# Kernel tuning notes

Measured on AMD Instinct MI355X. Metric: run time of the kernel, lower is better.

The kernel has to match this reference:

```python
import jax, jax.numpy as jnp
import numpy as np
import math

B, T, D_MODEL, H = 2, 2048, 768, 12
D = D_MODEL // H
EPS = 1e-8


def _l2norm(x, eps=EPS):
    # torch.nn.functional.normalize: x / max(||x||, eps)
    n = jnp.sqrt(jnp.sum(x * x, axis=-1, keepdims=True))
    return x / jnp.maximum(n, eps)


def setup_inputs() -> dict:
    key = jax.random.key(0)
    ks = jax.random.split(key, 7)
    sc = 1.0 / math.sqrt(D_MODEL)
    inp = {
        "query": jax.random.normal(ks[0], (B, T, D_MODEL), jnp.float32),
        "key": jax.random.normal(ks[1], (B, T, D_MODEL), jnp.float32),
        "value": jax.random.normal(ks[2], (B, T, D_MODEL), jnp.float32),
        "Wq": jax.random.normal(ks[3], (D_MODEL, D_MODEL), jnp.float32) * sc,
        "Wk": jax.random.normal(ks[4], (D_MODEL, D_MODEL), jnp.float32) * sc,
        "Wv": jax.random.normal(ks[5], (D_MODEL, D_MODEL), jnp.float32) * sc,
        "Wo": jax.random.normal(ks[6], (D_MODEL, D_MODEL), jnp.float32) * sc,
        "s_v": jnp.linspace(0.0, math.log(255.0), H).astype(jnp.float32),
        "s_r": jnp.zeros((H,), jnp.float32),
    }
    return inp


def reference(query, key, value, Wq, Wk, Wv, Wo, s_v, s_r):
    b, t, _ = query.shape

    def proj(x, W):  # Linear(bias=False) then split heads -> [B,H,T,D]
        return (x @ W.T).reshape(b, t, H, D).transpose(0, 2, 1, 3)

    q = _l2norm(proj(query, Wq))
    k = _l2norm(proj(key, Wk))
    v = _l2norm(proj(value, Wv))

    w = jnp.exp(s_v) + 1.0  # per-head decay exponent, in [2, 256]
    r = jnp.exp(s_r) + 1.0  # per-head scale

    # cosine-similarity scores in [-1, 1]
    s = jnp.einsum("bhqd,bhkd->bhqk", q, k)
    base = jnp.clip((s + 1.0) * 0.5, 0.0, 1.0)
    alpha = r[None, :, None, None] * jnp.power(base, w[None, :, None, None])

    # causal mask (no softmax normalization in screening attention)
    causal = jnp.tril(jnp.ones((t, t), dtype=bool))
    alpha = jnp.where(causal[None, None], alpha, 0.0)

    out = jnp.einsum("bhqk,bhkd->bhqd", alpha, v)  # [B,H,T,D]

    # TanhNorm: bound magnitude along head dim via tanh of the norm
    n = jnp.sqrt(jnp.sum(out * out, axis=-1, keepdims=True))
    out = jnp.tanh(n) * out / (n + EPS)

    out = out.transpose(0, 2, 1, 3).reshape(b, t, D_MODEL)
    return out @ Wo.T
```

## Files before the change

### kernel.cpp

```cpp
#include <hip/hip_runtime.h>
#include <hip/hip_bf16.h>
#include <math.h>


typedef __attribute__((ext_vector_type(8))) short short8;
typedef __attribute__((ext_vector_type(4))) float f32x4;
typedef __attribute__((ext_vector_type(4))) unsigned int uint4v;
typedef __attribute__((ext_vector_type(2))) unsigned int uint2v;
typedef __attribute__((ext_vector_type(4))) float float4v;

#define MFMA_BF16(a, b, c) __builtin_amdgcn_mfma_f32_16x16x32_bf16((a), (b), (c), 0, 0, 0)

static __device__ __forceinline__ unsigned short f2bf(float f) {
  union { float f; unsigned u; } v; v.f = f;
  unsigned r = v.u + 0x7FFFu + ((v.u >> 16) & 1u);
  return (unsigned short)(r >> 16);
}
static __device__ __forceinline__ unsigned pack2(float a, float b) {
  return (unsigned)f2bf(a) | ((unsigned)f2bf(b) << 16);
}
static __device__ __forceinline__ void gload_lds16(const void* g, void* l) {
  __builtin_amdgcn_global_load_lds((const __attribute__((address_space(1))) unsigned int*)g,
                                   (__attribute__((address_space(3))) unsigned int*)l, 16, 0, 0);
}

__global__ __launch_bounds__(256) void k_cvt(
    const float* __restrict__ s0, const float* __restrict__ s1, const float* __restrict__ s2,
    const float* __restrict__ s3, const float* __restrict__ s4, const float* __restrict__ s5,
    const float* __restrict__ s6, unsigned short* __restrict__ dst) {
  const size_t e = ((size_t)blockIdx.x * 256 + threadIdx.x) * 8;
  const float* src;
  size_t off;
  if (e < 9437184) {
    const int i = (int)(e / 3145728);
    src = (i == 0) ? s0 : (i == 1) ? s1 : s2;
    off = e - (size_t)i * 3145728;
  } else {
    const size_t ew = e - 9437184;
    const int i = (int)(ew / 589824);
    src = (i == 0) ? s3 : (i == 1) ? s4 : (i == 2) ? s5 : s6;
    off = ew - (size_t)i * 589824;
  }
  const float4v f0 = *(const float4v*)(src + off);
  const float4v f1 = *(const float4v*)(src + off + 4);
  uint4v u = {pack2(f0.x, f0.y), pack2(f0.z, f0.w), pack2(f1.x, f1.y), pack2(f1.z, f1.w)};
  *(uint4v*)(dst + e) = u;
}

__global__ __launch_bounds__(512) void k_proj(
    const unsigned short* __restrict__ Xb, const unsigned short* __restrict__ Wb,
    unsigned short* __restrict__ qb, unsigned short* __restrict__ kb,
    unsigned short* __restrict__ vtb) {
  __shared__ alignas(16) unsigned char smem[49152];
  float* o_s = (float*)smem;
  unsigned short* vt_s = (unsigned short*)smem;

  const int which = blockIdx.z;
  const int h = blockIdx.y;
  const unsigned short* X = Xb + (size_t)which * 3145728;
  const unsigned short* W = Wb + (size_t)which * 589824 + (size_t)h * 64 * 768;

  const int mbase = blockIdx.x * 128;
  const int tid = threadIdx.x;
  const int lane = tid & 63;
  const int wv = tid >> 6;
  const int wm = wv >> 1, wn = wv & 1;
  const int l15 = lane & 15, l4 = lane >> 4;
  const int srow8 = lane >> 3;
  const int schunk = (lane & 7) ^ srow8;

  f32x4 acc[2][2];
#pragma unroll
  for (int m = 0; m < 2; ++m)
#pragma unroll
    for (int n = 0; n < 2; ++n) acc[m][n] = (f32x4){0.f, 0.f, 0.f, 0.f};

#pragma unroll
  for (int i = 0; i < 2; ++i) {
    const int j = wv * 2 + i;
    gload_lds16(X + (size_t)(mbase + j * 8 + srow8) * 768 + schunk * 8, smem + j * 1024);
  }
  gload_lds16(W + (size_t)(wv * 8 + srow8) * 768 + schunk * 8, smem + 16384 + wv * 1024);

  for (int ks = 0; ks < 12; ++ks) {
    const int cur = (ks & 1) * 24576;
    asm volatile("s_waitcnt vmcnt(0)" ::: "memory");
    __builtin_amdgcn_sched_barrier(0);
    __builtin_amdgcn_s_barrier();
    __builtin_amdgcn_sched_barrier(0);
    if (ks < 11) {
      const int nxt = ((ks + 1) & 1) * 24576;
      const int k0n = (ks + 1) * 64;
#pragma unroll
      for (int i = 0; i < 2; ++i) {
        const int j = wv * 2 + i;
        gload_lds16(X + (size_t)(mbase + j * 8 + srow8) * 768 + k0n + schunk * 8,
                    smem + nxt + j * 1024);
      }
      gload_lds16(W + (size_t)(wv * 8 + srow8) * 768 + k0n + schunk * 8,
                  smem + nxt + 16384 + wv * 1024);
      __builtin_amdgcn_sched_barrier(0);
    }
    __builtin_amdgcn_s_setprio(1);
#pragma unroll
    for (int kc = 0; kc < 2; ++kc) {
      const int cx = (kc << 2) | l4;
      short8 ar[2], br[2];
#pragma unroll
      for (int m = 0; m < 2; ++m) {
        const int r = wm * 32 + m * 16 + l15;
        ar[m] = *(const short8*)(smem + cur + r * 128 + ((cx ^ (r & 7)) << 4));
      }
#pragma unroll
      for (int n = 0; n < 2; ++n) {
        const int r = wn * 32 + n * 16 + l15;
        br[n] = *(const short8*)(smem + cur + 16384 + r * 128 + ((cx ^ (r & 7)) << 4));
      }
#pragma unroll
      for (int m = 0; m < 2; ++m)
#pragma unroll
        for (int n = 0; n < 2; ++n) acc[m][n] = MFMA_BF16(ar[m], br[n], acc[m][n]);
    }
    __builtin_amdgcn_s_setprio(0);
  }

  const int b = mbase >> 11;
  const int tbase = mbase & 2047;
  const int bh = b * 12 + h;
  __syncthreads();
#pragma unroll
  for (int m = 0; m < 2; ++m)
#pragma unroll
    for (int n = 0; n < 2; ++n)
#pragma unroll
      for (int j = 0; j < 4; ++j)
        o_s[(wm * 32 + m * 16 + l4 * 4 + j) * 68 + wn * 32 + n * 16 + l15] = acc[m][n][j];
  __syncthreads();
  const int row2 = tid >> 2, q4 = tid & 3;
  float v[16];
  float ss = 0.f;
#pragma unroll
  for (int c = 0; c < 4; ++c) {
    float4v f = *(const float4v*)(o_s + row2 * 68 + q4 * 16 + c * 4);
    v[c * 4 + 0] = f.x; v[c * 4 + 1] = f.y; v[c * 4 + 2] = f.z; v[c * 4 + 3] = f.w;
    ss += f.x * f.x + f.y * f.y + f.z * f.z + f.w * f.w;
  }
  ss += __shfl_xor(ss, 1);
  ss += __shfl_xor(ss, 2);
  const float inv = 1.f / fmaxf(sqrtf(ss), 1e-8f);
  if (which < 2) {
    unsigned short* outp =
        ((which == 0) ? qb : kb) + ((size_t)bh * 2048 + tbase + row2) * 64 + q4 * 16;
    uint4v o0 = {pack2(v[0] * inv, v[1] * inv), pack2(v[2] * inv, v[3] * inv),
                 pack2(v[4] * inv, v[5] * inv), pack2(v[6] * inv, v[7] * inv)};
    uint4v o1 = {pack2(v[8] * inv, v[9] * inv), pack2(v[10] * inv, v[11] * inv),
                 pack2(v[12] * inv, v[13] * inv), pack2(v[14] * inv, v[15] * inv)};
    *(uint4v*)(outp) = o0;
    *(uint4v*)(outp + 8) = o1;
  } else {
    __syncthreads();
#pragma unroll
    for (int c = 0; c < 16; ++c)
      vt_s[(q4 * 16 + c) * 136 + row2] = f2bf(v[c] * inv);
    __syncthreads();
    const int d = tid >> 3, tc = (tid & 7) * 16;
    unsigned short* dst = vtb + ((size_t)bh * 64 + d) * 2048 + tbase + tc;
    *(uint4v*)(dst) = *(const uint4v*)(vt_s + d * 136 + tc);
    *(uint4v*)(dst + 8) = *(const uint4v*)(vt_s + d * 136 + tc + 8);
  }
}

__global__ __launch_bounds__(512) void k_attn(
    const unsigned short* __restrict__ qb, const unsigned short* __restrict__ kb,
    const unsigned short* __restrict__ vtb, const float* __restrict__ s_v,
    const float* __restrict__ s_r, unsigned short* __restrict__ attn) {
  __shared__ alignas(16) unsigned char smem[41984];
  unsigned short* p_s = (unsigned short*)(smem + 32768);
  float* o_s = (float*)smem;

  const int bid = blockIdx.x;
  const int ii = bid & 255, jj = bid >> 8;
  const int rank = (jj == 0) ? ii : (jj == 1) ? (511 - ii) : (512 + ii);
  const int qt = 31 - (rank / 24);
  const int bh = rank % 24;
  const int b = bh / 12, h = bh % 12;
  const int qbase = qt * 64;
  const unsigned short* Qp = qb + (size_t)bh * 2048 * 64;
  const unsigned short* Kp = kb + (size_t)bh * 2048 * 64;
  const unsigned short* VTp = vtb + (size_t)bh * 64 * 2048;

  const int tid = threadIdx.x;
  const int lane = tid & 63;
  const int wv = tid >> 6;
  const int wm = wv >> 2, wn = wv & 3;
  const int l15 = lane & 15, l4 = lane >> 4;
  const int srow8 = lane >> 3;
  const int schunk = (lane & 7) ^ srow8;

  const float w_h = expf(s_v[h]) + 1.0f;
  const float lr_h = log2f(expf(s_r[h]) + 1.0f);

  gload_lds16(Kp + (size_t)(wv * 8 + srow8) * 64 + schunk * 8, smem + wv * 1024);
  gload_lds16(VTp + (size_t)(wv * 8 + srow8) * 2048 + schunk * 8, smem + 16384 + wv * 1024);

  short8 qf[2];
#pragma unroll
  for (int kc = 0; kc < 2; ++kc)
    qf[kc] = *(const short8*)(Qp + (size_t)(qbase + wn * 16 + l15) * 64 + kc * 32 + l4 * 8);

  f32x4 acc_o[2];
#pragma unroll
  for (int m = 0; m < 2; ++m) acc_o[m] = (f32x4){0.f, 0.f, 0.f, 0.f};

  for (int kt = 0; kt <= qt; ++kt) {
    const int cur = (kt & 1) * 8192;
    asm volatile("s_waitcnt vmcnt(0)" ::: "memory");
    __builtin_amdgcn_sched_barrier(0);
    __builtin_amdgcn_s_barrier();
    __builtin_amdgcn_sched_barrier(0);
    if (kt < qt) {
      const int nxt = ((kt + 1) & 1) * 8192;
      const int kb2 = (kt + 1) * 64;
      gload_lds16(Kp + (size_t)(kb2 + wv * 8 + srow8) * 64 + schunk * 8, smem + nxt + wv * 1024);
      gload_lds16(VTp + (size_t)(wv * 8 + srow8) * 2048 + kb2 + schunk * 8,
                  smem + 16384 + nxt + wv * 1024);
      __builtin_amdgcn_sched_barrier(0);
    }
    f32x4 s_acc[2];
#pragma unroll
    for (int m = 0; m < 2; ++m) s_acc[m] = (f32x4){0.f, 0.f, 0.f, 0.f};
    __builtin_amdgcn_s_setprio(1);
#pragma unroll
    for (int kc = 0; kc < 2; ++kc) {
      const int cx = (kc << 2) | l4;
      const int r0 = wm * 32 + l15, r1 = wm * 32 + 16 + l15;
      short8 a0 = *(const short8*)(smem + cur + r0 * 128 + ((cx ^ (r0 & 7)) << 4));
      short8 a1 = *(const short8*)(smem + cur + r1 * 128 + ((cx ^ (r1 & 7)) << 4));
      s_acc[0] = MFMA_BF16(a0, qf[kc], s_acc[0]);
      s_acc[1] = MFMA_BF16(a1, qf[kc], s_acc[1]);
    }
    __builtin_amdgcn_s_setprio(0);
    const bool diag = (kt == qt);
#pragma unroll
    for (int m = 0; m < 2; ++m) {
      const int lkb = wm * 32 + m * 16 + l4 * 4;
      const int lq = wn * 16 + l15;
      float av[4];
#pragma unroll
      for (int t = 0; t < 4; ++t) {
        const float base = __builtin_amdgcn_fmed3f(fmaf(s_acc[m][t], 0.5f, 0.5f), 0.f, 1.f);
        float a = __builtin_amdgcn_exp2f(fmaf(w_h, __builtin_amdgcn_logf(base), lr_h));
        if (diag && (lkb + t) > lq) a = 0.f;
        av[t] = a;
      }
      uint2v u = {pack2(av[0], av[1]), pack2(av[2], av[3])};
      *(uint2v*)(p_s + lq * 72 + lkb) = u;
    }
    asm volatile("s_waitcnt lgkmcnt(0)" ::: "memory");
    __builtin_amdgcn_sched_barrier(0);
    __builtin_amdgcn_s_barrier();
    __builtin_amdgcn_sched_barrier(0);
    __builtin_amdgcn_s_setprio(1);
#pragma unroll
    for (int kc = 0; kc < 2; ++kc) {
      const int cx = (kc << 2) | l4;
      const int r0 = wm * 32 + l15, r1 = wm * 32 + 16 + l15;
      short8 pa = *(const short8*)(p_s + (wn * 16 + l15) * 72 + kc * 32 + l4 * 8);
      short8 vb0 = *(const short8*)(smem + 16384 + cur + r0 * 128 + ((cx ^ (r0 & 7)) << 4));
      short8 vb1 = *(const short8*)(smem + 16384 + cur + r1 * 128 + ((cx ^ (r1 & 7)) << 4));
      acc_o[0] = MFMA_BF16(pa, vb0, acc_o[0]);
      acc_o[1] = MFMA_BF16(pa, vb1, acc_o[1]);
    }
    __builtin_amdgcn_s_setprio(0);
  }
  __syncthreads();
#pragma unroll
  for (int m = 0; m < 2; ++m)
#pragma unroll
    for (int j = 0; j < 4; ++j)
      o_s[(wn * 16 + l4 * 4 + j) * 68 + wm * 32 + m * 16 + l15] = acc_o[m][j];
  __syncthreads();
  {
    const int row = tid >> 3, d8 = (tid & 7) * 8;
    float vals[8];
    float ss = 0.f;
#pragma unroll
    for (int c = 0; c < 2; ++c) {
      float4v f = *(const float4v*)(o_s + row * 68 + d8 + c * 4);
      vals[c * 4 + 0] = f.x; vals[c * 4 + 1] = f.y; vals[c * 4 + 2] = f.z; vals[c * 4 + 3] = f.w;
      ss += f.x * f.x + f.y * f.y + f.z * f.z + f.w * f.w;
    }
    ss += __shfl_xor(ss, 1);
    ss += __shfl_xor(ss, 2);
    ss += __shfl_xor(ss, 4);
    const float nrm = sqrtf(ss);
    const float sc = tanhf(nrm) / (nrm + 1e-8f);
    unsigned short* dst = attn + (size_t)(b * 2048 + qbase + row) * 768 + h * 64 + d8;
    uint4v o = {pack2(vals[0] * sc, vals[1] * sc), pack2(vals[2] * sc, vals[3] * sc),
                pack2(vals[4] * sc, vals[5] * sc), pack2(vals[6] * sc, vals[7] * sc)};
    *(uint4v*)(dst) = o;
  }
}

__global__ __launch_bounds__(512) void k_outproj(const unsigned short* __restrict__ attn,
                                                 const unsigned short* __restrict__ Wob,
                                                 float* __restrict__ out) {
  __shared__ alignas(16) unsigned char smem[49152];
  const int mbase = blockIdx.x * 128;
  const int nbase = blockIdx.y * 64;
  const int tid = threadIdx.x;
  const int lane = tid & 63;
  const int wv = tid >> 6;
  const int wm = wv >> 1, wn = wv & 1;
  const int l15 = lane & 15, l4 = lane >> 4;
  const int srow8 = lane >> 3;
  const int schunk = (lane & 7) ^ srow8;

  f32x4 acc[2][2];
#pragma unroll
  for (int m = 0; m < 2; ++m)
#pragma unroll
    for (int n = 0; n < 2; ++n) acc[m][n] = (f32x4){0.f, 0.f, 0.f, 0.f};

#pragma unroll
  for (int i = 0; i < 2; ++i) {
    const int j = wv * 2 + i;
    gload_lds16(attn + (size_t)(mbase + j * 8 + srow8) * 768 + schunk * 8, smem + j * 1024);
  }
  gload_lds16(Wob + (size_t)(nbase + wv * 8 + srow8) * 768 + schunk * 8,
              smem + 16384 + wv * 1024);

  for (int ks = 0; ks < 12; ++ks) {
    const int cur = (ks & 1) * 24576;
    asm volatile("s_waitcnt vmcnt(0)" ::: "memory");
    __builtin_amdgcn_sched_barrier(0);
    __builtin_amdgcn_s_barrier();
    __builtin_amdgcn_sched_barrier(0);
    if (ks < 11) {
      const int nxt = ((ks + 1) & 1) * 24576;
      const int k0n = (ks + 1) * 64;
#pragma unroll
      for (int i = 0; i < 2; ++i) {
        const int j = wv * 2 + i;
        gload_lds16(attn + (size_t)(mbase + j * 8 + srow8) * 768 + k0n + schunk * 8,
                    smem + nxt + j * 1024);
      }
      gload_lds16(Wob + (size_t)(nbase + wv * 8 + srow8) * 768 + k0n + schunk * 8,
                  smem + nxt + 16384 + wv * 1024);
      __builtin_amdgcn_sched_barrier(0);
    }
    __builtin_amdgcn_s_setprio(1);
#pragma unroll
    for (int kc = 0; kc < 2; ++kc) {
      const int cx = (kc << 2) | l4;
      short8 ar[2], br[2];
#pragma unroll
      for (int m = 0; m < 2; ++m) {
        const int r = wm * 32 + m * 16 + l15;
        ar[m] = *(const short8*)(smem + cur + r * 128 + ((cx ^ (r & 7)) << 4));
      }
#pragma unroll
      for (int n = 0; n < 2; ++n) {
        const int r = wn * 32 + n * 16 + l15;
        br[n] = *(const short8*)(smem + cur + 16384 + r * 128 + ((cx ^ (r & 7)) << 4));
      }
#pragma unroll
      for (int m = 0; m < 2; ++m)
#pragma unroll
        for (int n = 0; n < 2; ++n) acc[m][n] = MFMA_BF16(ar[m], br[n], acc[m][n]);
    }
    __builtin_amdgcn_s_setprio(0);
  }
#pragma unroll
  for (int m = 0; m < 2; ++m)
#pragma unroll
    for (int n = 0; n < 2; ++n)
#pragma unroll
      for (int j = 0; j < 4; ++j)
        out[(size_t)(mbase + wm * 32 + m * 16 + l4 * 4 + j) * 768 + nbase + wn * 32 + n * 16 +
            l15] = acc[m][n][j];
}

extern "C" void kernel_launch(void* const* d_in, const int* in_sizes, int n_in, void* d_out,
                              int out_size, void* d_ws, size_t ws_size, hipStream_t stream) {
  (void)in_sizes;
  (void)n_in;
  (void)out_size;
  (void)ws_size;
  const float* query = (const float*)d_in[0];
  const float* key = (const float*)d_in[1];
  const float* value = (const float*)d_in[2];
  const float* Wq = (const float*)d_in[3];
  const float* Wk = (const float*)d_in[4];
  const float* Wv = (const float*)d_in[5];
  const float* Wo = (const float*)d_in[6];
  const float* s_v = (const float*)d_in[7];
  const float* s_r = (const float*)d_in[8];
  float* out = (float*)d_out;

  unsigned short* cvt = (unsigned short*)d_ws;
  unsigned short* Xb = cvt;
  unsigned short* Wb = cvt + 9437184;
  unsigned short* qb = cvt + 11796480;
  unsigned short* kb = qb + 3145728;
  unsigned short* vtb = kb + 3145728;
  unsigned short* attn = cvt;

  k_cvt<<<5760, 256, 0, stream>>>(query, key, value, Wq, Wk, Wv, Wo, cvt);
  k_proj<<<dim3(32, 12, 3), 512, 0, stream>>>(Xb, Wb, qb, kb, vtb);
  k_attn<<<dim3(768), 512, 0, stream>>>(qb, kb, vtb, s_v, s_r, attn);
  k_outproj<<<dim3(32, 12), 512, 0, stream>>>(attn, Wb + 3 * 589824, out);
}
```

Before: 79.76 us.

## Split PV over key halves per wave to drop the mid-loop barrier

The PV product is reorganized so each wave uses only the P columns it wrote itself (its key half wm) and covers all 64 head dims with transposed accumulators. This lets the block-wide barrier between writing P and reading it be removed. The two key-half partial outputs are then summed through shared memory at the end, which costs an extra barrier pass and more accumulator registers. Correctness relies on each wave reading only P entries from its own writes, which the layout appears to ensure.

```diff
diff --git a/kernel.cpp b/kernel.cpp
--- a/kernel.cpp
+++ b/kernel.cpp
@@ -208,9 +208,9 @@
   for (int kc = 0; kc < 2; ++kc)
     qf[kc] = *(const short8*)(Qp + (size_t)(qbase + wn * 16 + l15) * 64 + kc * 32 + l4 * 8);
 
-  f32x4 acc_o[2];
-#pragma unroll
-  for (int m = 0; m < 2; ++m) acc_o[m] = (f32x4){0.f, 0.f, 0.f, 0.f};
+  f32x4 acc_oT[4];
+#pragma unroll
+  for (int g = 0; g < 4; ++g) acc_oT[g] = (f32x4){0.f, 0.f, 0.f, 0.f};
 
   for (int kt = 0; kt <= qt; ++kt) {
     const int cur = (kt & 1) * 8192;
@@ -258,27 +258,35 @@
     }
     asm volatile("s_waitcnt lgkmcnt(0)" ::: "memory");
     __builtin_amdgcn_sched_barrier(0);
-    __builtin_amdgcn_s_barrier();
-    __builtin_amdgcn_sched_barrier(0);
     __builtin_amdgcn_s_setprio(1);
-#pragma unroll
-    for (int kc = 0; kc < 2; ++kc) {
-      const int cx = (kc << 2) | l4;
-      const int r0 = wm * 32 + l15, r1 = wm * 32 + 16 + l15;
-      short8 pa = *(const short8*)(p_s + (wn * 16 + l15) * 72 + kc * 32 + l4 * 8);
-      short8 vb0 = *(const short8*)(smem + 16384 + cur + r0 * 128 + ((cx ^ (r0 & 7)) << 4));
-      short8 vb1 = *(const short8*)(smem + 16384 + cur + r1 * 128 + ((cx ^ (r1 & 7)) << 4));
-      acc_o[0] = MFMA_BF16(pa, vb0, acc_o[0]);
-      acc_o[1] = MFMA_BF16(pa, vb1, acc_o[1]);
+    {
+      short8 pb = *(const short8*)(p_s + (wn * 16 + l15) * 72 + wm * 32 + l4 * 8);
+#pragma unroll
+      for (int dg = 0; dg < 4; ++dg) {
+        const int rd = dg * 16 + l15;
+        short8 va = *(const short8*)(smem + 16384 + cur + rd * 128 +
+                                     (((wm * 4 + l4) ^ (rd & 7)) << 4));
+        acc_oT[dg] = MFMA_BF16(va, pb, acc_oT[dg]);
+      }
     }
     __builtin_amdgcn_s_setprio(0);
   }
   __syncthreads();
-#pragma unroll
-  for (int m = 0; m < 2; ++m)
-#pragma unroll
-    for (int j = 0; j < 4; ++j)
-      o_s[(wn * 16 + l4 * 4 + j) * 68 + wm * 32 + m * 16 + l15] = acc_o[m][j];
+  if (wm == 0) {
+#pragma unroll
+    for (int dg = 0; dg < 4; ++dg)
+#pragma unroll
+      for (int j = 0; j < 4; ++j)
+        o_s[(wn * 16 + l15) * 68 + dg * 16 + l4 * 4 + j] = acc_oT[dg][j];
+  }
+  __syncthreads();
+  if (wm == 1) {
+#pragma unroll
+    for (int dg = 0; dg < 4; ++dg)
+#pragma unroll
+      for (int j = 0; j < 4; ++j)
+        o_s[(wn * 16 + l15) * 68 + dg * 16 + l4 * 4 + j] += acc_oT[dg][j];
+  }
   __syncthreads();
   {
     const int row = tid >> 3, d8 = (tid & 7) * 8;
```

Result: faster. 77.17 us (-3.3%).
